# Optimization experiments

Measured on AMD Instinct MI355X. Metric: run time of the kernel, lower is better.

## Reference

```python
import jax, jax.numpy as jnp
import numpy as np

MESSAGE_SIZE = 128
MESSAGE_PASSES = 3
N_BONDS = 7      # Single, Double, Triple, Quadruple, Aromatic, Pi, Universal
N_LAYERS = 8     # 8 bias-free Linear layers, ReLU after the first 7
N_TYPES = 6      # top-4 ranked atoms + atom 0, plus catchall slot (index 5)
ATOM_VALS = [6.0, 7.0, 8.0, 9.0, 16.0, 17.0, 1.0]
TOP_ATOMS = [6.0, 7.0, 8.0, 9.0, 0.0]


def setup_inputs() -> dict:
    key = jax.random.key(0)
    ks = jax.random.split(key, 8)
    B, N, F, D = 128, 128, 75, MESSAGE_SIZE
    g = jax.random.uniform(ks[0], (B, N_BONDS, N, N), dtype=jnp.float32)
    h = jax.random.normal(ks[1], (B, N, F), dtype=jnp.float32)
    # channel 0 carries the atomic number used for GRU routing
    atom_ids = jax.random.randint(ks[2], (B, N), 0, len(ATOM_VALS))
    h = h.at[:, :, 0].set(jnp.asarray(ATOM_VALS, jnp.float32)[atom_ids])
    s = 1.0 / np.sqrt(D)
    msg_W = jax.random.normal(ks[3], (N_BONDS, N_LAYERS, D, D), jnp.float32) * s
    gru_Wih = jax.random.normal(ks[4], (2, N_TYPES, 3 * D, D), jnp.float32) * s  # [regular/universal, type, 3H, H]
    gru_Whh = jax.random.normal(ks[5], (2, N_TYPES, 3 * D, D), jnp.float32) * s
    gru_bih = jax.random.normal(ks[6], (2, N_TYPES, 3 * D), jnp.float32) * s
    gru_bhh = jax.random.normal(ks[7], (2, N_TYPES, 3 * D), jnp.float32) * s
    return dict(g=g, h=h, msg_W=msg_W, gru_Wih=gru_Wih, gru_Whh=gru_Whh,
                gru_bih=gru_bih, gru_bhh=gru_bhh)


def _gru_grouped(x, hx, tid, Wih, Whh, bih, bhh):
    """torch.nn.GRUCell(input=x, hx=hx) with per-node parameter group tid in [0,T).
    Wih/Whh: [T, 3H, H], bih/bhh: [T, 3H]."""
    gx = jnp.einsum('nd,tgd->ntg', x, Wih)   # [n, T, 3H]
    gh = jnp.einsum('nd,tgd->ntg', hx, Whh)
    gx = jnp.take_along_axis(gx, tid[:, None, None], axis=1)[:, 0] + bih[tid]
    gh = jnp.take_along_axis(gh, tid[:, None, None], axis=1)[:, 0] + bhh[tid]
    xr, xz, xn = jnp.split(gx, 3, axis=-1)
    hr, hz, hn = jnp.split(gh, 3, axis=-1)
    r = jax.nn.sigmoid(xr + hr)
    z = jax.nn.sigmoid(xz + hz)
    n = jnp.tanh(xn + r * hn)
    return (1.0 - z) * n + z * hx


def reference(g, h, msg_W, gru_Wih, gru_Whh, gru_bih, gru_bhh):
    B, N, F = h.shape
    D = msg_W.shape[-1]
    h_t = jnp.concatenate([h, jnp.zeros((B, N, D - F), h.dtype)], axis=2)  # [B,N,D]
    atoms = h[:, :, 0].reshape(-1)
    tid = jnp.full(atoms.shape, N_TYPES - 1, jnp.int32)  # default catchall
    for i, a in enumerate(TOP_ATOMS):
        tid = jnp.where(atoms == jnp.float32(a), jnp.int32(i), tid)
    for _ in range(MESSAGE_PASSES):
        # per-bond-type 8-layer bias-free MLP, vectorized over the 7 bond types
        xb = jnp.broadcast_to(h_t[None], (N_BONDS, B, N, D))
        for l in range(N_LAYERS):
            xb = jnp.einsum('kbnd,ked->kbne', xb, msg_W[:, l])
            if l < N_LAYERS - 1:
                xb = jax.nn.relu(xb)
        # bmm aggregation per bond type: m_k = g[:,k] @ xb_k
        m_all = jnp.einsum('bknm,kbmd->kbnd', g, xb)
        m_non = m_all[:N_BONDS - 1].sum(0).reshape(-1, D)
        m_uni = m_all[N_BONDS - 1].reshape(-1, D)
        h_flat = h_t.reshape(-1, D)
        out = _gru_grouped(h_flat, m_non, tid, gru_Wih[0], gru_Whh[0], gru_bih[0], gru_bhh[0])
        out_u = _gru_grouped(h_flat, m_uni, tid, gru_Wih[1], gru_Whh[1], gru_bih[1], gru_bhh[1])
        h_t = (out + out_u).reshape(B, N, D)
    return h_t
```

## Files before the change

kernel.cpp:

```cpp
#include <hip/hip_runtime.h>
#include <math.h>

#define NBOND 7
#define NLAY 8
#define NTYPE 6
#define NNODES 16384
#define PX 136

typedef _Float16 half8 __attribute__((ext_vector_type(8)));
typedef _Float16 half4 __attribute__((ext_vector_type(4)));
typedef float floatx16 __attribute__((ext_vector_type(16)));

__device__ __forceinline__ float sig_(float x) { return 1.0f / (1.0f + __expf(-x)); }
__device__ __forceinline__ int drow_(int reg, int hi) { return (reg & 3) + 8 * (reg >> 2) + 4 * hi; }

__device__ __forceinline__ _Float16 hi_(float v) { return (_Float16)v; }
__device__ __forceinline__ _Float16 lo_(float v) { return (_Float16)(v - (float)(_Float16)v); }

__global__ void setup_kernel(const float* __restrict__ h, float* __restrict__ hT,
                             int* __restrict__ counts, int* __restrict__ bucket)
{
    int gid = blockIdx.x * 256 + threadIdx.x;
    int node = gid >> 7, d = gid & 127;
    hT[gid] = (d < 75) ? h[node * 75 + d] : 0.0f;
    if (gid < NNODES) {
        float a = h[gid * 75];
        int tt = 5;
        if      (a == 6.0f) tt = 0;
        else if (a == 7.0f) tt = 1;
        else if (a == 8.0f) tt = 2;
        else if (a == 9.0f) tt = 3;
        else if (a == 0.0f) tt = 4;
        int slot = atomicAdd(&counts[tt], 1);
        bucket[tt * NNODES + slot] = gid;
    }
}

__global__ void pack_msg_kernel(const float* __restrict__ msgW, _Float16* __restrict__ Wp)
{
    int idx = blockIdx.x * 256 + threadIdx.x;
    if (idx >= NBOND * NLAY * 16 * 128) return;
    int e  = idx & 127;
    int c  = (idx >> 7) & 15;
    int kl = idx >> 11;
    const float* src = msgW + ((size_t)kl * 128 + e) * 128 + c * 8;
    float4 u = *(const float4*)src;
    float4 v = *(const float4*)(src + 4);
    float av[8] = {u.x, u.y, u.z, u.w, v.x, v.y, v.z, v.w};
    half8 hh, ll;
    #pragma unroll
    for (int j = 0; j < 8; ++j) { hh[j] = hi_(av[j]); ll[j] = lo_(av[j]); }
    _Float16* dst = Wp + ((size_t)kl * 16 + c) * 2048;
    *(half8*)(dst + e * 8)        = hh;
    *(half8*)(dst + 1024 + e * 8) = ll;
}

__global__ void pack_gru_kernel(const float* __restrict__ Wih, const float* __restrict__ Whh,
                                _Float16* __restrict__ Wp)
{
    int idx = blockIdx.x * 256 + threadIdx.x;
    if (idx >= 2 * NTYPE * 2 * 16 * 384) return;
    int col = idx % 384;
    int c   = (idx / 384) & 15;
    int vm  = idx / 6144;
    int mat = vm & 1;
    int vt  = vm >> 1;
    const float* src = (mat ? Whh : Wih) + ((size_t)vt * 384 + col) * 128 + c * 8;
    float4 u = *(const float4*)src;
    float4 v = *(const float4*)(src + 4);
    float av[8] = {u.x, u.y, u.z, u.w, v.x, v.y, v.z, v.w};
    half8 hh, ll;
    #pragma unroll
    for (int j = 0; j < 8; ++j) { hh[j] = hi_(av[j]); ll[j] = lo_(av[j]); }
    _Float16* dst = Wp + (size_t)vm * 98304 + (size_t)c * 6144;
    *(half8*)(dst + col * 8)        = hh;
    *(half8*)(dst + 3072 + col * 8) = ll;
}

__global__ __launch_bounds__(256) void mlp_agg_mfma(
    const float* __restrict__ hT, const _Float16* __restrict__ Wp,
    const float* __restrict__ gmat, float* __restrict__ m_non, float* __restrict__ m_uni)
{
    __shared__ _Float16 Xhi[128 * PX];
    __shared__ _Float16 Xlo[128 * PX];

    const int t = threadIdx.x;
    const int kb = blockIdx.x, b = blockIdx.y;
    const int wave = t >> 6, lane = t & 63, lo = lane & 31, hi = lane >> 5;
    const int row = wave * 32 + lo;

    for (int q = t; q < 128 * 32; q += 256) {
        int r = q >> 5, c4 = q & 31;
        float4 v = *(const float4*)(hT + ((size_t)(b * 128 + r)) * 128 + c4 * 4);
        half4 hh, ll;
        hh[0] = hi_(v.x); ll[0] = lo_(v.x);
        hh[1] = hi_(v.y); ll[1] = lo_(v.y);
        hh[2] = hi_(v.z); ll[2] = lo_(v.z);
        hh[3] = hi_(v.w); ll[3] = lo_(v.w);
        *(half4*)(Xhi + r * PX + c4 * 4) = hh;
        *(half4*)(Xlo + r * PX + c4 * 4) = ll;
    }
    __syncthreads();

    floatx16 acc[4];

    #pragma unroll 1
    for (int l = 0; l < NLAY; ++l) {
        #pragma unroll
        for (int ct = 0; ct < 4; ++ct) acc[ct] = (floatx16)0.0f;
        const _Float16* wb = Wp + ((size_t)(kb * NLAY + l) * 16) * 2048;

        #pragma unroll 2
        for (int kk = 0; kk < 8; ++kk) {
            half8 a_h = *(const half8*)(Xhi + row * PX + kk * 16 + hi * 8);
            half8 a_l = *(const half8*)(Xlo + row * PX + kk * 16 + hi * 8);
            const _Float16* bp = wb + (size_t)(kk * 2 + hi) * 2048;
            #pragma unroll
            for (int ct = 0; ct < 4; ++ct) {
                half8 b_h = *(const half8*)(bp + (ct * 32 + lo) * 8);
                half8 b_l = *(const half8*)(bp + 1024 + (ct * 32 + lo) * 8);
                acc[ct] = __builtin_amdgcn_mfma_f32_32x32x16_f16(a_h, b_h, acc[ct], 0, 0, 0);
                acc[ct] = __builtin_amdgcn_mfma_f32_32x32x16_f16(a_h, b_l, acc[ct], 0, 0, 0);
                acc[ct] = __builtin_amdgcn_mfma_f32_32x32x16_f16(a_l, b_h, acc[ct], 0, 0, 0);
            }
        }
        __syncthreads();

        if (l < NLAY - 1) {
            #pragma unroll
            for (int ct = 0; ct < 4; ++ct)
                #pragma unroll
                for (int reg = 0; reg < 16; ++reg) {
                    int n = wave * 32 + drow_(reg, hi);
                    float vv = fmaxf(acc[ct][reg], 0.0f);
                    Xhi[n * PX + ct * 32 + lo] = hi_(vv);
                    Xlo[n * PX + ct * 32 + lo] = lo_(vv);
                }
        } else {
            #pragma unroll
            for (int ct = 0; ct < 4; ++ct)
                #pragma unroll
                for (int s = 0; s < 4; ++s) {
                    int e = ct * 32 + lo, m0 = wave * 32 + 8 * s + 4 * hi;
                    half4 hh, ll;
                    #pragma unroll
                    for (int j = 0; j < 4; ++j) {
                        float vv = acc[ct][4 * s + j];
                        hh[j] = hi_(vv); ll[j] = lo_(vv);
                    }
                    *(half4*)(Xhi + e * PX + m0) = hh;
                    *(half4*)(Xlo + e * PX + m0) = ll;
                }
        }
        __syncthreads();
    }

    #pragma unroll
    for (int ct = 0; ct < 4; ++ct) acc[ct] = (floatx16)0.0f;
    const float* grow = gmat + (size_t)(b * NBOND + kb) * 16384;

    #pragma unroll 2
    for (int kk = 0; kk < 8; ++kk) {
        const float* gp = grow + (size_t)row * 128 + kk * 16 + hi * 8;
        float4 u = *(const float4*)gp, v2 = *(const float4*)(gp + 4);
        float av[8] = {u.x, u.y, u.z, u.w, v2.x, v2.y, v2.z, v2.w};
        half8 a_h, a_l;
        #pragma unroll
        for (int j = 0; j < 8; ++j) { a_h[j] = hi_(av[j]); a_l[j] = lo_(av[j]); }
        #pragma unroll
        for (int ct = 0; ct < 4; ++ct) {
            half8 b_h = *(const half8*)(Xhi + (ct * 32 + lo) * PX + kk * 16 + hi * 8);
            half8 b_l = *(const half8*)(Xlo + (ct * 32 + lo) * PX + kk * 16 + hi * 8);
            acc[ct] = __builtin_amdgcn_mfma_f32_32x32x16_f16(a_h, b_h, acc[ct], 0, 0, 0);
            acc[ct] = __builtin_amdgcn_mfma_f32_32x32x16_f16(a_h, b_l, acc[ct], 0, 0, 0);
            acc[ct] = __builtin_amdgcn_mfma_f32_32x32x16_f16(a_l, b_h, acc[ct], 0, 0, 0);
        }
    }

    if (kb == NBOND - 1) {
        #pragma unroll
        for (int ct = 0; ct < 4; ++ct)
            #pragma unroll
            for (int reg = 0; reg < 16; ++reg) {
                int n = wave * 32 + drow_(reg, hi);
                m_uni[((size_t)(b * 128 + n)) * 128 + ct * 32 + lo] = acc[ct][reg];
            }
    } else {
        #pragma unroll
        for (int ct = 0; ct < 4; ++ct)
            #pragma unroll
            for (int reg = 0; reg < 16; ++reg) {
                int n = wave * 32 + drow_(reg, hi);
                atomicAdd(m_non + ((size_t)(b * 128 + n)) * 128 + ct * 32 + lo, acc[ct][reg]);
            }
    }
}

__global__ __launch_bounds__(256) void gru_mfma(
    float* __restrict__ hT, const float* __restrict__ m_non, const float* __restrict__ m_uni,
    const int* __restrict__ counts, const int* __restrict__ bucket,
    const _Float16* __restrict__ Wp, const float* __restrict__ bihp, const float* __restrict__ bhhp)
{
    __shared__ _Float16 Xh[64 * PX], Xl[64 * PX], Mh[64 * PX], Ml[64 * PX];
    __shared__ int bl[64];

    const int t = threadIdx.x, tt = blockIdx.y;
    const int cnt  = counts[tt];
    const int base = blockIdx.x * 64;
    if (base >= cnt) return;
    const int nn = min(64, cnt - base);
    if (t < 64) bl[t] = (t < nn) ? bucket[tt * NNODES + base + t] : -1;
    __syncthreads();

    const int wave = t >> 6, lane = t & 63, lo = lane & 31, hi = lane >> 5;
    const int d = wave * 32 + lo;

    for (int q = t; q < 64 * 32; q += 256) {
        int r = q >> 5, c4 = q & 31;
        float4 v = make_float4(0.f, 0.f, 0.f, 0.f);
        int node = bl[r];
        if (node >= 0) v = *(const float4*)(hT + (size_t)node * 128 + c4 * 4);
        half4 hh, ll;
        hh[0] = hi_(v.x); ll[0] = lo_(v.x);
        hh[1] = hi_(v.y); ll[1] = lo_(v.y);
        hh[2] = hi_(v.z); ll[2] = lo_(v.z);
        hh[3] = hi_(v.w); ll[3] = lo_(v.w);
        *(half4*)(Xh + r * PX + c4 * 4) = hh;
        *(half4*)(Xl + r * PX + c4 * 4) = ll;
    }

    #pragma unroll 1
    for (int rt = 0; rt < 2; ++rt) {
        float hacc[16];
        #pragma unroll
        for (int reg = 0; reg < 16; ++reg) hacc[reg] = 0.0f;
        const int rrow = rt * 32 + lo;

        #pragma unroll 1
        for (int v = 0; v < 2; ++v) {
            const float* msrc = v ? m_uni : m_non;
            __syncthreads();
            for (int q = t; q < 64 * 32; q += 256) {
                int r = q >> 5, c4 = q & 31;
                float4 mv = make_float4(0.f, 0.f, 0.f, 0.f);
                int node = bl[r];
                if (node >= 0) mv = *(const float4*)(msrc + (size_t)node * 128 + c4 * 4);
                half4 hh, ll;
                hh[0] = hi_(mv.x); ll[0] = lo_(mv.x);
                hh[1] = hi_(mv.y); ll[1] = lo_(mv.y);
                hh[2] = hi_(mv.z); ll[2] = lo_(mv.z);
                hh[3] = hi_(mv.w); ll[3] = lo_(mv.w);
                *(half4*)(Mh + r * PX + c4 * 4) = hh;
                *(half4*)(Ml + r * PX + c4 * 4) = ll;
            }
            __syncthreads();

            const int vt = v * NTYPE + tt;
            const _Float16* pih = Wp + (size_t)(vt * 2 + 0) * 98304;
            const _Float16* phh = Wp + (size_t)(vt * 2 + 1) * 98304;

            floatx16 ar = (floatx16)0.0f, az = (floatx16)0.0f;
            floatx16 ax = (floatx16)0.0f, ah = (floatx16)0.0f;

            #pragma unroll 2
            for (int kk = 0; kk < 8; ++kk) {
                int koff = kk * 16 + hi * 8;
                half8 xh = *(const half8*)(Xh + rrow * PX + koff);
                half8 xl = *(const half8*)(Xl + rrow * PX + koff);
                half8 mh = *(const half8*)(Mh + rrow * PX + koff);
                half8 ml = *(const half8*)(Ml + rrow * PX + koff);
                const _Float16* ci = pih + (size_t)(kk * 2 + hi) * 6144;
                const _Float16* ch = phh + (size_t)(kk * 2 + hi) * 6144;
                half8 birh = *(const half8*)(ci + (0   + d) * 8);
                half8 birl = *(const half8*)(ci + 3072 + (0   + d) * 8);
                half8 bizh = *(const half8*)(ci + (128 + d) * 8);
                half8 bizl = *(const half8*)(ci + 3072 + (128 + d) * 8);
                half8 binh = *(const half8*)(ci + (256 + d) * 8);
                half8 binl = *(const half8*)(ci + 3072 + (256 + d) * 8);
                half8 bhrh = *(const half8*)(ch + (0   + d) * 8);
                half8 bhrl = *(const half8*)(ch + 3072 + (0   + d) * 8);
                half8 bhzh = *(const half8*)(ch + (128 + d) * 8);
                half8 bhzl = *(const half8*)(ch + 3072 + (128 + d) * 8);
                half8 bhnh = *(const half8*)(ch + (256 + d) * 8);
                half8 bhnl = *(const half8*)(ch + 3072 + (256 + d) * 8);

                ar = __builtin_amdgcn_mfma_f32_32x32x16_f16(xh, birh, ar, 0, 0, 0);
                ar = __builtin_amdgcn_mfma_f32_32x32x16_f16(xh, birl, ar, 0, 0, 0);
                ar = __builtin_amdgcn_mfma_f32_32x32x16_f16(xl, birh, ar, 0, 0, 0);
                ar = __builtin_amdgcn_mfma_f32_32x32x16_f16(mh, bhrh, ar, 0, 0, 0);
                ar = __builtin_amdgcn_mfma_f32_32x32x16_f16(mh, bhrl, ar, 0, 0, 0);
                ar = __builtin_amdgcn_mfma_f32_32x32x16_f16(ml, bhrh, ar, 0, 0, 0);

                az = __builtin_amdgcn_mfma_f32_32x32x16_f16(xh, bizh, az, 0, 0, 0);
                az = __builtin_amdgcn_mfma_f32_32x32x16_f16(xh, bizl, az, 0, 0, 0);
                az = __builtin_amdgcn_mfma_f32_32x32x16_f16(xl, bizh, az, 0, 0, 0);
                az = __builtin_amdgcn_mfma_f32_32x32x16_f16(mh, bhzh, az, 0, 0, 0);
                az = __builtin_amdgcn_mfma_f32_32x32x16_f16(mh, bhzl, az, 0, 0, 0);
                az = __builtin_amdgcn_mfma_f32_32x32x16_f16(ml, bhzh, az, 0, 0, 0);

                ax = __builtin_amdgcn_mfma_f32_32x32x16_f16(xh, binh, ax, 0, 0, 0);
                ax = __builtin_amdgcn_mfma_f32_32x32x16_f16(xh, binl, ax, 0, 0, 0);
                ax = __builtin_amdgcn_mfma_f32_32x32x16_f16(xl, binh, ax, 0, 0, 0);
                ah = __builtin_amdgcn_mfma_f32_32x32x16_f16(mh, bhnh, ah, 0, 0, 0);
                ah = __builtin_amdgcn_mfma_f32_32x32x16_f16(mh, bhnl, ah, 0, 0, 0);
                ah = __builtin_amdgcn_mfma_f32_32x32x16_f16(ml, bhnh, ah, 0, 0, 0);
            }

            const float* bi = bihp + (size_t)vt * 384;
            const float* bh = bhhp + (size_t)vt * 384;
            float b_r  = bi[d] + bh[d];
            float b_z  = bi[128 + d] + bh[128 + d];
            float b_in = bi[256 + d];
            float b_hn = bh[256 + d];
            #pragma unroll
            for (int reg = 0; reg < 16; ++reg) {
                int n = rt * 32 + drow_(reg, hi);
                int node = bl[n];
                float r  = sig_(ar[reg] + b_r);
                float z  = sig_(az[reg] + b_z);
                float nv = tanhf(ax[reg] + b_in + r * (ah[reg] + b_hn));
                float mv = (node >= 0) ? msrc[(size_t)node * 128 + d] : 0.0f;
                hacc[reg] += (1.0f - z) * nv + z * mv;
            }
        }

        #pragma unroll
        for (int reg = 0; reg < 16; ++reg) {
            int n = rt * 32 + drow_(reg, hi);
            int node = bl[n];
            if (node >= 0) hT[(size_t)node * 128 + d] = hacc[reg];
        }
    }
}

extern "C" void kernel_launch(void* const* d_in, const int* in_sizes, int n_in,
                              void* d_out, int out_size, void* d_ws, size_t ws_size,
                              hipStream_t stream) {
    const float* g    = (const float*)d_in[0];
    const float* h    = (const float*)d_in[1];
    const float* msgW = (const float*)d_in[2];
    const float* Wih  = (const float*)d_in[3];
    const float* Whh  = (const float*)d_in[4];
    const float* bih  = (const float*)d_in[5];
    const float* bhh  = (const float*)d_in[6];
    float* hT = (float*)d_out;

    char* ws = (char*)d_ws;
    float* m_non = (float*)ws;
    float* m_uni = m_non + (size_t)NNODES * 128;
    int* counts  = (int*)(ws + 2 * (size_t)NNODES * 128 * 4);
    int* bucket  = counts + 8;
    _Float16* WpM = (_Float16*)(bucket + NTYPE * NNODES);
    _Float16* WpG = WpM + (size_t)NBOND * NLAY * 16 * 2048;

    (void)hipMemsetAsync(counts, 0, 8 * sizeof(int), stream);
    setup_kernel<<<NNODES * 128 / 256, 256, 0, stream>>>(h, hT, counts, bucket);
    pack_msg_kernel<<<(NBOND * NLAY * 16 * 128 + 255) / 256, 256, 0, stream>>>(msgW, WpM);
    pack_gru_kernel<<<(2 * NTYPE * 2 * 16 * 384 + 255) / 256, 256, 0, stream>>>(Wih, Whh, WpG);

    for (int pass = 0; pass < 3; ++pass) {
        (void)hipMemsetAsync(m_non, 0, (size_t)NNODES * 128 * 4, stream);
        mlp_agg_mfma<<<dim3(NBOND, 128), 256, 0, stream>>>(hT, WpM, g, m_non, m_uni);
        gru_mfma<<<dim3(NNODES / 64, NTYPE), 256, 0, stream>>>(hT, m_non, m_uni, counts, bucket,
                                                               WpG, bih, bhh);
    }
}
```

Measured before the change: 948.9 us.

## Split GRU blocks by variant and row tile, use ping-pong buffers and atomic output

The GRU kernel grid gains a z dimension that spreads the regular/universal variant and the 32-row tile across separate blocks, where each block used to loop over both. Each block now stages only its own 32 nodes and its message rows in shared memory. Partial GRU outputs are combined with atomicAdd into a zeroed output buffer, and input and output ping-pong between two h buffers so blocks never read what others write. Separately, the MLP kernel drops the block barriers around the ReLU layer writeback, because each wave only reads and writes its own rows. The gain in parallelism and occupancy (launch bounds set to 3) comes at the cost of an extra memset per pass, float atomics on the output, and a workspace buffer for the second h copy.

```diff
diff --git a/kernel.cpp b/kernel.cpp
--- a/kernel.cpp
+++ b/kernel.cpp
@@ -78,7 +78,7 @@
 }
 
 __global__ __launch_bounds__(256) void mlp_agg_mfma(
-    const float* __restrict__ hT, const _Float16* __restrict__ Wp,
+    const float* __restrict__ hin, const _Float16* __restrict__ Wp,
     const float* __restrict__ gmat, float* __restrict__ m_non, float* __restrict__ m_uni)
 {
     __shared__ _Float16 Xhi[128 * PX];
@@ -91,7 +91,7 @@
 
     for (int q = t; q < 128 * 32; q += 256) {
         int r = q >> 5, c4 = q & 31;
-        float4 v = *(const float4*)(hT + ((size_t)(b * 128 + r)) * 128 + c4 * 4);
+        float4 v = *(const float4*)(hin + ((size_t)(b * 128 + r)) * 128 + c4 * 4);
         half4 hh, ll;
         hh[0] = hi_(v.x); ll[0] = lo_(v.x);
         hh[1] = hi_(v.y); ll[1] = lo_(v.y);
@@ -124,7 +124,6 @@
                 acc[ct] = __builtin_amdgcn_mfma_f32_32x32x16_f16(a_l, b_h, acc[ct], 0, 0, 0);
             }
         }
-        __syncthreads();
 
         if (l < NLAY - 1) {
             #pragma unroll
@@ -137,6 +136,7 @@
                     Xlo[n * PX + ct * 32 + lo] = lo_(vv);
                 }
         } else {
+            __syncthreads();
             #pragma unroll
             for (int ct = 0; ct < 4; ++ct)
                 #pragma unroll
@@ -151,8 +151,8 @@
                     *(half4*)(Xhi + e * PX + m0) = hh;
                     *(half4*)(Xlo + e * PX + m0) = ll;
                 }
+            __syncthreads();
         }
-        __syncthreads();
     }
 
     #pragma unroll
@@ -196,140 +196,120 @@
     }
 }
 
-__global__ __launch_bounds__(256) void gru_mfma(
-    float* __restrict__ hT, const float* __restrict__ m_non, const float* __restrict__ m_uni,
+__global__ __launch_bounds__(256, 3) void gru_mfma(
+    const float* __restrict__ hin, float* __restrict__ hout,
+    const float* __restrict__ m_non, const float* __restrict__ m_uni,
     const int* __restrict__ counts, const int* __restrict__ bucket,
     const _Float16* __restrict__ Wp, const float* __restrict__ bihp, const float* __restrict__ bhhp)
 {
-    __shared__ _Float16 Xh[64 * PX], Xl[64 * PX], Mh[64 * PX], Ml[64 * PX];
-    __shared__ int bl[64];
+    __shared__ _Float16 Xh[32 * PX], Xl[32 * PX], Mh[32 * PX], Ml[32 * PX];
+    __shared__ int bl[32];
 
     const int t = threadIdx.x, tt = blockIdx.y;
+    const int v = blockIdx.z >> 1, rtile = blockIdx.z & 1;
     const int cnt  = counts[tt];
-    const int base = blockIdx.x * 64;
+    const int base = blockIdx.x * 64 + rtile * 32;
     if (base >= cnt) return;
-    const int nn = min(64, cnt - base);
-    if (t < 64) bl[t] = (t < nn) ? bucket[tt * NNODES + base + t] : -1;
+    const int nn = min(32, cnt - base);
+    if (t < 32) bl[t] = (t < nn) ? bucket[tt * NNODES + base + t] : -1;
+    __syncthreads();
+
+    const float* msrc = v ? m_uni : m_non;
+
+    for (int q = t; q < 32 * 32; q += 256) {
+        int r = q >> 5, c4 = q & 31;
+        float4 xv = make_float4(0.f, 0.f, 0.f, 0.f);
+        float4 mv = make_float4(0.f, 0.f, 0.f, 0.f);
+        int node = bl[r];
+        if (node >= 0) {
+            xv = *(const float4*)(hin  + (size_t)node * 128 + c4 * 4);
+            mv = *(const float4*)(msrc + (size_t)node * 128 + c4 * 4);
+        }
+        half4 hh, ll;
+        hh[0] = hi_(xv.x); ll[0] = lo_(xv.x);
+        hh[1] = hi_(xv.y); ll[1] = lo_(xv.y);
+        hh[2] = hi_(xv.z); ll[2] = lo_(xv.z);
+        hh[3] = hi_(xv.w); ll[3] = lo_(xv.w);
+        *(half4*)(Xh + r * PX + c4 * 4) = hh;
+        *(half4*)(Xl + r * PX + c4 * 4) = ll;
+        hh[0] = hi_(mv.x); ll[0] = lo_(mv.x);
+        hh[1] = hi_(mv.y); ll[1] = lo_(mv.y);
+        hh[2] = hi_(mv.z); ll[2] = lo_(mv.z);
+        hh[3] = hi_(mv.w); ll[3] = lo_(mv.w);
+        *(half4*)(Mh + r * PX + c4 * 4) = hh;
+        *(half4*)(Ml + r * PX + c4 * 4) = ll;
+    }
     __syncthreads();
 
     const int wave = t >> 6, lane = t & 63, lo = lane & 31, hi = lane >> 5;
     const int d = wave * 32 + lo;
-
-    for (int q = t; q < 64 * 32; q += 256) {
-        int r = q >> 5, c4 = q & 31;
-        float4 v = make_float4(0.f, 0.f, 0.f, 0.f);
-        int node = bl[r];
-        if (node >= 0) v = *(const float4*)(hT + (size_t)node * 128 + c4 * 4);
-        half4 hh, ll;
-        hh[0] = hi_(v.x); ll[0] = lo_(v.x);
-        hh[1] = hi_(v.y); ll[1] = lo_(v.y);
-        hh[2] = hi_(v.z); ll[2] = lo_(v.z);
-        hh[3] = hi_(v.w); ll[3] = lo_(v.w);
-        *(half4*)(Xh + r * PX + c4 * 4) = hh;
-        *(half4*)(Xl + r * PX + c4 * 4) = ll;
-    }
-
-    #pragma unroll 1
-    for (int rt = 0; rt < 2; ++rt) {
-        float hacc[16];
-        #pragma unroll
-        for (int reg = 0; reg < 16; ++reg) hacc[reg] = 0.0f;
-        const int rrow = rt * 32 + lo;
-
-        #pragma unroll 1
-        for (int v = 0; v < 2; ++v) {
-            const float* msrc = v ? m_uni : m_non;
-            __syncthreads();
-            for (int q = t; q < 64 * 32; q += 256) {
-                int r = q >> 5, c4 = q & 31;
-                float4 mv = make_float4(0.f, 0.f, 0.f, 0.f);
-                int node = bl[r];
-                if (node >= 0) mv = *(const float4*)(msrc + (size_t)node * 128 + c4 * 4);
-                half4 hh, ll;
-                hh[0] = hi_(mv.x); ll[0] = lo_(mv.x);
-                hh[1] = hi_(mv.y); ll[1] = lo_(mv.y);
-                hh[2] = hi_(mv.z); ll[2] = lo_(mv.z);
-                hh[3] = hi_(mv.w); ll[3] = lo_(mv.w);
-                *(half4*)(Mh + r * PX + c4 * 4) = hh;
-                *(half4*)(Ml + r * PX + c4 * 4) = ll;
-            }
-            __syncthreads();
-
-            const int vt = v * NTYPE + tt;
-            const _Float16* pih = Wp + (size_t)(vt * 2 + 0) * 98304;
-            const _Float16* phh = Wp + (size_t)(vt * 2 + 1) * 98304;
-
-            floatx16 ar = (floatx16)0.0f, az = (floatx16)0.0f;
-            floatx16 ax = (floatx16)0.0f, ah = (floatx16)0.0f;
-
-            #pragma unroll 2
-            for (int kk = 0; kk < 8; ++kk) {
-                int koff = kk * 16 + hi * 8;
-                half8 xh = *(const half8*)(Xh + rrow * PX + koff);
-                half8 xl = *(const half8*)(Xl + rrow * PX + koff);
-                half8 mh = *(const half8*)(Mh + rrow * PX + koff);
-                half8 ml = *(const half8*)(Ml + rrow * PX + koff);
-                const _Float16* ci = pih + (size_t)(kk * 2 + hi) * 6144;
-                const _Float16* ch = phh + (size_t)(kk * 2 + hi) * 6144;
-                half8 birh = *(const half8*)(ci + (0   + d) * 8);
-                half8 birl = *(const half8*)(ci + 3072 + (0   + d) * 8);
-                half8 bizh = *(const half8*)(ci + (128 + d) * 8);
-                half8 bizl = *(const half8*)(ci + 3072 + (128 + d) * 8);
-                half8 binh = *(const half8*)(ci + (256 + d) * 8);
-                half8 binl = *(const half8*)(ci + 3072 + (256 + d) * 8);
-                half8 bhrh = *(const half8*)(ch + (0   + d) * 8);
-                half8 bhrl = *(const half8*)(ch + 3072 + (0   + d) * 8);
-                half8 bhzh = *(const half8*)(ch + (128 + d) * 8);
-                half8 bhzl = *(const half8*)(ch + 3072 + (128 + d) * 8);
-                half8 bhnh = *(const half8*)(ch + (256 + d) * 8);
-                half8 bhnl = *(const half8*)(ch + 3072 + (256 + d) * 8);
-
-                ar = __builtin_amdgcn_mfma_f32_32x32x16_f16(xh, birh, ar, 0, 0, 0);
-                ar = __builtin_amdgcn_mfma_f32_32x32x16_f16(xh, birl, ar, 0, 0, 0);
-                ar = __builtin_amdgcn_mfma_f32_32x32x16_f16(xl, birh, ar, 0, 0, 0);
-                ar = __builtin_amdgcn_mfma_f32_32x32x16_f16(mh, bhrh, ar, 0, 0, 0);
-                ar = __builtin_amdgcn_mfma_f32_32x32x16_f16(mh, bhrl, ar, 0, 0, 0);
-                ar = __builtin_amdgcn_mfma_f32_32x32x16_f16(ml, bhrh, ar, 0, 0, 0);
-
-                az = __builtin_amdgcn_mfma_f32_32x32x16_f16(xh, bizh, az, 0, 0, 0);
-                az = __builtin_amdgcn_mfma_f32_32x32x16_f16(xh, bizl, az, 0, 0, 0);
-                az = __builtin_amdgcn_mfma_f32_32x32x16_f16(xl, bizh, az, 0, 0, 0);
-                az = __builtin_amdgcn_mfma_f32_32x32x16_f16(mh, bhzh, az, 0, 0, 0);
-                az = __builtin_amdgcn_mfma_f32_32x32x16_f16(mh, bhzl, az, 0, 0, 0);
-                az = __builtin_amdgcn_mfma_f32_32x32x16_f16(ml, bhzh, az, 0, 0, 0);
-
-                ax = __builtin_amdgcn_mfma_f32_32x32x16_f16(xh, binh, ax, 0, 0, 0);
-                ax = __builtin_amdgcn_mfma_f32_32x32x16_f16(xh, binl, ax, 0, 0, 0);
-                ax = __builtin_amdgcn_mfma_f32_32x32x16_f16(xl, binh, ax, 0, 0, 0);
-                ah = __builtin_amdgcn_mfma_f32_32x32x16_f16(mh, bhnh, ah, 0, 0, 0);
-                ah = __builtin_amdgcn_mfma_f32_32x32x16_f16(mh, bhnl, ah, 0, 0, 0);
-                ah = __builtin_amdgcn_mfma_f32_32x32x16_f16(ml, bhnh, ah, 0, 0, 0);
-            }
-
-            const float* bi = bihp + (size_t)vt * 384;
-            const float* bh = bhhp + (size_t)vt * 384;
-            float b_r  = bi[d] + bh[d];
-            float b_z  = bi[128 + d] + bh[128 + d];
-            float b_in = bi[256 + d];
-            float b_hn = bh[256 + d];
-            #pragma unroll
-            for (int reg = 0; reg < 16; ++reg) {
-                int n = rt * 32 + drow_(reg, hi);
-                int node = bl[n];
-                float r  = sig_(ar[reg] + b_r);
-                float z  = sig_(az[reg] + b_z);
-                float nv = tanhf(ax[reg] + b_in + r * (ah[reg] + b_hn));
-                float mv = (node >= 0) ? msrc[(size_t)node * 128 + d] : 0.0f;
-                hacc[reg] += (1.0f - z) * nv + z * mv;
-            }
-        }
-
-        #pragma unroll
-        for (int reg = 0; reg < 16; ++reg) {
-            int n = rt * 32 + drow_(reg, hi);
-            int node = bl[n];
-            if (node >= 0) hT[(size_t)node * 128 + d] = hacc[reg];
-        }
+    const int vt = v * NTYPE + tt;
+    const _Float16* pih = Wp + (size_t)(vt * 2 + 0) * 98304;
+    const _Float16* phh = Wp + (size_t)(vt * 2 + 1) * 98304;
+
+    floatx16 ar = (floatx16)0.0f, az = (floatx16)0.0f;
+    floatx16 ax = (floatx16)0.0f, ah = (floatx16)0.0f;
+
+    #pragma unroll 2
+    for (int kk = 0; kk < 8; ++kk) {
+        int koff = kk * 16 + hi * 8;
+        half8 xh = *(const half8*)(Xh + lo * PX + koff);
+        half8 xl = *(const half8*)(Xl + lo * PX + koff);
+        half8 mh = *(const half8*)(Mh + lo * PX + koff);
+        half8 ml = *(const half8*)(Ml + lo * PX + koff);
+        const _Float16* ci = pih + (size_t)(kk * 2 + hi) * 6144;
+        const _Float16* ch = phh + (size_t)(kk * 2 + hi) * 6144;
+        half8 birh = *(const half8*)(ci + (0   + d) * 8);
+        half8 birl = *(const half8*)(ci + 3072 + (0   + d) * 8);
+        half8 bizh = *(const half8*)(ci + (128 + d) * 8);
+        half8 bizl = *(const half8*)(ci + 3072 + (128 + d) * 8);
+        half8 binh = *(const half8*)(ci + (256 + d) * 8);
+        half8 binl = *(const half8*)(ci + 3072 + (256 + d) * 8);
+        half8 bhrh = *(const half8*)(ch + (0   + d) * 8);
+        half8 bhrl = *(const half8*)(ch + 3072 + (0   + d) * 8);
+        half8 bhzh = *(const half8*)(ch + (128 + d) * 8);
+        half8 bhzl = *(const half8*)(ch + 3072 + (128 + d) * 8);
+        half8 bhnh = *(const half8*)(ch + (256 + d) * 8);
+        half8 bhnl = *(const half8*)(ch + 3072 + (256 + d) * 8);
+
+        ar = __builtin_amdgcn_mfma_f32_32x32x16_f16(xh, birh, ar, 0, 0, 0);
+        ar = __builtin_amdgcn_mfma_f32_32x32x16_f16(xh, birl, ar, 0, 0, 0);
+        ar = __builtin_amdgcn_mfma_f32_32x32x16_f16(xl, birh, ar, 0, 0, 0);
+        ar = __builtin_amdgcn_mfma_f32_32x32x16_f16(mh, bhrh, ar, 0, 0, 0);
+        ar = __builtin_amdgcn_mfma_f32_32x32x16_f16(mh, bhrl, ar, 0, 0, 0);
+        ar = __builtin_amdgcn_mfma_f32_32x32x16_f16(ml, bhrh, ar, 0, 0, 0);
+
+        az = __builtin_amdgcn_mfma_f32_32x32x16_f16(xh, bizh, az, 0, 0, 0);
+        az = __builtin_amdgcn_mfma_f32_32x32x16_f16(xh, bizl, az, 0, 0, 0);
+        az = __builtin_amdgcn_mfma_f32_32x32x16_f16(xl, bizh, az, 0, 0, 0);
+        az = __builtin_amdgcn_mfma_f32_32x32x16_f16(mh, bhzh, az, 0, 0, 0);
+        az = __builtin_amdgcn_mfma_f32_32x32x16_f16(mh, bhzl, az, 0, 0, 0);
+        az = __builtin_amdgcn_mfma_f32_32x32x16_f16(ml, bhzh, az, 0, 0, 0);
+
+        ax = __builtin_amdgcn_mfma_f32_32x32x16_f16(xh, binh, ax, 0, 0, 0);
+        ax = __builtin_amdgcn_mfma_f32_32x32x16_f16(xh, binl, ax, 0, 0, 0);
+        ax = __builtin_amdgcn_mfma_f32_32x32x16_f16(xl, binh, ax, 0, 0, 0);
+        ah = __builtin_amdgcn_mfma_f32_32x32x16_f16(mh, bhnh, ah, 0, 0, 0);
+        ah = __builtin_amdgcn_mfma_f32_32x32x16_f16(mh, bhnl, ah, 0, 0, 0);
+        ah = __builtin_amdgcn_mfma_f32_32x32x16_f16(ml, bhnh, ah, 0, 0, 0);
+    }
+
+    const float* bi = bihp + (size_t)vt * 384;
+    const float* bh = bhhp + (size_t)vt * 384;
+    float b_r  = bi[d] + bh[d];
+    float b_z  = bi[128 + d] + bh[128 + d];
+    float b_in = bi[256 + d];
+    float b_hn = bh[256 + d];
+    #pragma unroll
+    for (int reg = 0; reg < 16; ++reg) {
+        int n = drow_(reg, hi);
+        int node = bl[n];
+        if (node < 0) continue;
+        float r  = sig_(ar[reg] + b_r);
+        float z  = sig_(az[reg] + b_z);
+        float nv = tanhf(ax[reg] + b_in + r * (ah[reg] + b_hn));
+        float mv = msrc[(size_t)node * 128 + d];
+        atomicAdd(hout + (size_t)node * 128 + d, (1.0f - z) * nv + z * mv);
     }
 }
 
@@ -343,7 +323,7 @@
     const float* Whh  = (const float*)d_in[4];
     const float* bih  = (const float*)d_in[5];
     const float* bhh  = (const float*)d_in[6];
-    float* hT = (float*)d_out;
+    float* h1 = (float*)d_out;
 
     char* ws = (char*)d_ws;
     float* m_non = (float*)ws;
@@ -352,16 +332,21 @@
     int* bucket  = counts + 8;
     _Float16* WpM = (_Float16*)(bucket + NTYPE * NNODES);
     _Float16* WpG = WpM + (size_t)NBOND * NLAY * 16 * 2048;
+    float* h0 = (float*)(WpG + (size_t)2 * NTYPE * 2 * 98304);
 
     (void)hipMemsetAsync(counts, 0, 8 * sizeof(int), stream);
-    setup_kernel<<<NNODES * 128 / 256, 256, 0, stream>>>(h, hT, counts, bucket);
+    setup_kernel<<<NNODES * 128 / 256, 256, 0, stream>>>(h, h0, counts, bucket);
     pack_msg_kernel<<<(NBOND * NLAY * 16 * 128 + 255) / 256, 256, 0, stream>>>(msgW, WpM);
     pack_gru_kernel<<<(2 * NTYPE * 2 * 16 * 384 + 255) / 256, 256, 0, stream>>>(Wih, Whh, WpG);
 
+    const float* hin_p[3]  = {h0, h1, h0};
+    float*       hout_p[3] = {h1, h0, h1};
     for (int pass = 0; pass < 3; ++pass) {
         (void)hipMemsetAsync(m_non, 0, (size_t)NNODES * 128 * 4, stream);
-        mlp_agg_mfma<<<dim3(NBOND, 128), 256, 0, stream>>>(hT, WpM, g, m_non, m_uni);
-        gru_mfma<<<dim3(NNODES / 64, NTYPE), 256, 0, stream>>>(hT, m_non, m_uni, counts, bucket,
-                                                               WpG, bih, bhh);
-    }
-}
+        (void)hipMemsetAsync(hout_p[pass], 0, (size_t)NNODES * 128 * 4, stream);
+        mlp_agg_mfma<<<dim3(NBOND, 128), 256, 0, stream>>>(hin_p[pass], WpM, g, m_non, m_uni);
+        gru_mfma<<<dim3(NNODES / 64, NTYPE, 4), 256, 0, stream>>>(hin_p[pass], hout_p[pass],
+                                                                  m_non, m_uni, counts, bucket,
+                                                                  WpG, bih, bhh);
+    }
+}
```

Measured after the change: 908.2 us. 4.3% less time.
